# Performance work log

Hardware: AMD Instinct MI355X
Metric: run time of the kernel (lower is better)

Reference implementation:

```python
import jax, jax.numpy as jnp
import numpy as np

D = 256                      # covariance dim, hardcoded by bottleneck Conv2d(_, 256, 1)
ITER_N = 5                   # SqrtmLayer(output, 5)
_r, _c = np.triu_indices(D)
FLAT_IDX = jnp.asarray(_r * D + _c)   # upper-tri (incl. diag) indices into flattened d*d


def setup_inputs() -> dict:
    key = jax.random.key(0)
    ks = jax.random.split(key, 5)
    B, C, H, W = 64, 2048, 16, 16
    num_classes = 4
    feats = D * (D + 1) // 2  # 32896
    return {
        "features": jax.random.normal(ks[0], (B, C, H, W), jnp.float32),
        "w_bn": jax.random.normal(ks[1], (D, C), jnp.float32) * 0.02,
        "b_bn": jnp.zeros((D,), jnp.float32),
        "w_type": jax.random.normal(ks[2], (num_classes, feats), jnp.float32) * 0.01,
        "b_type": jnp.zeros((num_classes,), jnp.float32),
        "w_flag": jax.random.normal(ks[3], (1, feats), jnp.float32) * 0.01,
        "b_flag": jnp.zeros((1,), jnp.float32),
    }


def _covpool(x):
    # x: [B, d, h, w] -> second-order pooling: x_f @ I_hat @ x_f^T, equivalent
    # to (1/M) * centered @ centered^T  (I_hat = -1/M^2 * ones + 1/M * eye)
    B, d, h, w = x.shape
    M = h * w
    xf = x.reshape(B, d, M)
    centered = xf - xf.mean(axis=2, keepdims=True)
    return jnp.einsum('bim,bjm->bij', centered, centered) / M  # [B, d, d]


def _sqrtm_ns(A, iter_n=ITER_N):
    # Newton-Schulz iteration for matrix square root (iSQRT-COV style)
    B, d, _ = A.shape
    I3 = 3.0 * jnp.eye(d, dtype=A.dtype)
    normA = jnp.trace(A, axis1=1, axis2=2)          # [B], pre-normalization
    An = A / normA[:, None, None]
    ZY = 0.5 * (I3 - An)
    Y = jnp.matmul(An, ZY)
    Z = ZY
    for _ in range(iter_n - 2):
        ZY = 0.5 * (I3 - jnp.matmul(Z, Y))
        Y = jnp.matmul(Y, ZY)
        Z = jnp.matmul(ZY, Z)
    YZY = 0.5 * jnp.matmul(Y, I3 - jnp.matmul(Z, Y))
    return YZY * jnp.sqrt(normA)[:, None, None]     # post-compensation


def reference(features, w_bn, b_bn, w_type, b_type, w_flag, b_flag):
    # 1x1 bottleneck conv: [B, C, H, W] -> [B, 256, H, W]
    x = jnp.einsum('bchw,oc->bohw', features, w_bn) + b_bn[None, :, None, None]
    cov = _covpool(x)                # [B, 256, 256]
    s = _sqrtm_ns(cov)               # [B, 256, 256]
    B = s.shape[0]
    vec = s.reshape(B, D * D)[:, FLAT_IDX]   # triu-vec: [B, 32896]
    type_logits = vec @ w_type.T + b_type    # [B, num_classes]
    flag_logits = vec @ w_flag.T + b_flag    # [B, 1]
    return (type_logits, flag_logits)
```

## Files before the change

kernel.cpp:

```cpp
#include <hip/hip_runtime.h>
#include <math.h>


typedef __attribute__((ext_vector_type(8))) short bf16x8;
typedef __attribute__((ext_vector_type(4))) float f32x4;
typedef __attribute__((ext_vector_type(4))) unsigned u32x4;
typedef __attribute__((ext_vector_type(2))) unsigned u32x2;

enum { E_T = 0, E_TNS = 1, E_COV = 2, E_SF32 = 3 };

__device__ __forceinline__ unsigned fbits(float f) { union { float f; unsigned u; } x; x.f = f; return x.u; }
__device__ __forceinline__ float bitsf(unsigned u) { union { float f; unsigned u; } x; x.u = u; return x.f; }
__device__ __forceinline__ float bf16v(short h) { return bitsf(((unsigned)(unsigned short)h) << 16); }

__device__ __forceinline__ unsigned pack_h(float a, float b) {
  return (fbits(a) >> 16) | (fbits(b) & 0xFFFF0000u);
}
__device__ __forceinline__ unsigned pack_l(float a, float b) {
  float la = a - bitsf(fbits(a) & 0xFFFF0000u);
  float lb = b - bitsf(fbits(b) & 0xFFFF0000u);
  return (fbits(la) >> 16) | (fbits(lb) & 0xFFFF0000u);
}

__device__ __forceinline__ void gld16(const void* g, void* l) {
  __builtin_amdgcn_global_load_lds(
      (const __attribute__((address_space(1))) void*)(size_t)(g),
      (__attribute__((address_space(3))) void*)(unsigned)(size_t)(l), 16, 0, 0);
}

#define WAIT_VM(N) asm volatile("s_waitcnt vmcnt(" #N ")" ::: "memory")
#define BARRIER() do { __builtin_amdgcn_s_barrier(); asm volatile("" ::: "memory"); } while (0)

__global__ __launch_bounds__(256) void conv_k(
    const char* __restrict__ Wf, const float* __restrict__ F,
    char* __restrict__ X, const float* __restrict__ bias)
{
  __shared__ __align__(16) char lds[3 * 16384];
  const int tid = threadIdx.x, lane = tid & 63, w = tid >> 6;
  const int wr = w >> 1, wc = w & 1, fr = lane & 15, g = lane >> 4;
  const int bz = blockIdx.z, ib = blockIdx.y * 128, jb = blockIdx.x * 64;
  const float* Fb = F + (size_t)bz * 524288;

  f32x4 acc[4][2] = {};
  float xv[16];

  auto stageA = [&](int t) {
    const char* Ag = Wf + (size_t)t * 32768 + (size_t)ib * 128;
    char* lA = lds + (t % 3) * 16384;
#pragma unroll
    for (int i = 0; i < 4; ++i)
      gld16(Ag + (w + i * 4) * 1024 + lane * 16, lA + (w + i * 4) * 1024);
  };
  auto loadB = [&](int t) {
    const float* src = Fb + ((size_t)t * 32 + g * 8) * 256 + jb + wc * 32 + fr;
#pragma unroll
    for (int n = 0; n < 2; ++n)
#pragma unroll
      for (int e = 0; e < 8; ++e)
        xv[n * 8 + e] = src[e * 256 + n * 16];
  };

  stageA(0); stageA(1); loadB(0);

  for (int t = 0; t < 64; ++t) {
    if (t < 63) { WAIT_VM(20); } else { WAIT_VM(0); }
    BARRIER();
    if (t + 2 < 64) stageA(t + 2);
    bf16x8 bH[2], bL[2];
#pragma unroll
    for (int n = 0; n < 2; ++n) {
      short hh[8], ll[8];
#pragma unroll
      for (int e = 0; e < 8; ++e) {
        const float v = xv[n * 8 + e];
        const unsigned u = fbits(v);
        hh[e] = (short)(u >> 16);
        ll[e] = (short)(fbits(v - bitsf(u & 0xFFFF0000u)) >> 16);
      }
      bH[n] = *(bf16x8*)hh; bL[n] = *(bf16x8*)ll;
    }
    if (t + 1 < 64) loadB(t + 1);
    const char* lA = lds + (t % 3) * 16384;
    bf16x8 aH[4], aL[4];
#pragma unroll
    for (int m = 0; m < 4; ++m) {
      const int r = wr * 64 + m * 16 + fr;
      const char* p = lA + r * 128;
      aH[m] = *(const bf16x8*)(p + ((g ^ (r & 7)) << 4));
      aL[m] = *(const bf16x8*)(p + (((g + 4) ^ (r & 7)) << 4));
    }
#pragma unroll
    for (int m = 0; m < 4; ++m)
#pragma unroll
      for (int n = 0; n < 2; ++n) {
        f32x4 c = acc[m][n];
        c = __builtin_amdgcn_mfma_f32_16x16x32_bf16(aL[m], bH[n], c, 0, 0, 0);
        c = __builtin_amdgcn_mfma_f32_16x16x32_bf16(aH[m], bL[n], c, 0, 0, 0);
        c = __builtin_amdgcn_mfma_f32_16x16x32_bf16(aH[m], bH[n], c, 0, 0, 0);
        acc[m][n] = c;
      }
  }

  char* Xb = X + (size_t)bz * 262144;
#pragma unroll
  for (int m = 0; m < 4; ++m) {
    const int gi0 = ib + wr * 64 + m * 16 + g * 4;
#pragma unroll
    for (int n = 0; n < 2; ++n) {
      const int gj = jb + wc * 32 + n * 16 + fr;
      const int ktj = gj >> 5, sj = (gj & 31) >> 3, bo = (gj & 7) * 2;
#pragma unroll
      for (int j = 0; j < 4; ++j) {
        const int gi = gi0 + j;
        char* rp = Xb + (size_t)ktj * 32768 + (size_t)gi * 128;
        const float v = acc[m][n][j] + bias[gi];
        const unsigned u = fbits(v);
        *(short*)(rp + ((sj ^ (gi & 7)) << 4) + bo) = (short)(u >> 16);
        *(short*)(rp + (((sj + 4) ^ (gi & 7)) << 4) + bo) =
            (short)(fbits(v - bitsf(u & 0xFFFF0000u)) >> 16);
      }
    }
  }
}

template <int EPI, bool PAIR>
__global__ __launch_bounds__(128) void gemm_s(
    const char* __restrict__ A1, const char* __restrict__ B1, char* __restrict__ C1,
    const char* __restrict__ A2, const char* __restrict__ B2, char* __restrict__ C2,
    char* __restrict__ Cz, const float* __restrict__ mu,
    const float* __restrict__ nrm, float* __restrict__ Cf)
{
  static const int TIa[10] = {0, 0, 0, 0, 1, 1, 1, 2, 2, 3};
  static const int TJa[10] = {0, 1, 2, 3, 1, 2, 3, 2, 3, 3};
  __shared__ __align__(16) char lds[3 * 16384];
  const int tid = threadIdx.x, lane = tid & 63, w = tid >> 6;
  const int fr = lane & 15, g = lane >> 4;
  int bz = blockIdx.z;
  const char* Ab; const char* Bb; char* Cb;
  if (PAIR && bz >= 64) { bz -= 64; Ab = A2; Bb = B2; Cb = C2; }
  else { Ab = A1; Bb = B1; Cb = C1; }
  Ab += (size_t)bz * 262144; Bb += (size_t)bz * 262144; Cb += (size_t)bz * 262144;
  const int bi = TIa[blockIdx.x], bj = TJa[blockIdx.x];
  const int ib = bi * 64, jb = bj * 64;

  f32x4 acc[4][2] = {};

  auto stage = [&](int t) {
    char* lA = lds + (t % 3) * 16384;
    const char* Ag = Ab + (size_t)t * 32768 + (size_t)ib * 128;
    const char* Bg = Bb + (size_t)t * 32768 + (size_t)jb * 128;
#pragma unroll
    for (int i = 0; i < 8; ++i) {
      const int s = w + i * 2;
      if (s < 8) gld16(Ag + s * 1024 + lane * 16, lA + s * 1024);
      else       gld16(Bg + (s - 8) * 1024 + lane * 16, lA + 8192 + (s - 8) * 1024);
    }
  };

  stage(0); stage(1);
  for (int t = 0; t < 8; ++t) {
    if (t < 7) { WAIT_VM(8); } else { WAIT_VM(0); }
    BARRIER();
    if (t + 2 < 8) stage(t + 2);
    const char* lA = lds + (t % 3) * 16384;
    const char* lB = lA + 8192;
    bf16x8 aH[4], aL[4], bH[2], bL[2];
#pragma unroll
    for (int m = 0; m < 4; ++m) {
      const int r = m * 16 + fr;
      const char* p = lA + r * 128;
      aH[m] = *(const bf16x8*)(p + ((g ^ (r & 7)) << 4));
      aL[m] = *(const bf16x8*)(p + (((g + 4) ^ (r & 7)) << 4));
    }
#pragma unroll
    for (int n = 0; n < 2; ++n) {
      const int r = w * 32 + n * 16 + fr;
      const char* p = lB + r * 128;
      bH[n] = *(const bf16x8*)(p + ((g ^ (r & 7)) << 4));
      bL[n] = *(const bf16x8*)(p + (((g + 4) ^ (r & 7)) << 4));
    }
#pragma unroll
    for (int m = 0; m < 4; ++m)
#pragma unroll
      for (int n = 0; n < 2; ++n) {
        f32x4 c = acc[m][n];
        c = __builtin_amdgcn_mfma_f32_16x16x32_bf16(aL[m], bH[n], c, 0, 0, 0);
        c = __builtin_amdgcn_mfma_f32_16x16x32_bf16(aH[m], bL[n], c, 0, 0, 0);
        c = __builtin_amdgcn_mfma_f32_16x16x32_bf16(aH[m], bH[n], c, 0, 0, 0);
        acc[m][n] = c;
      }
  }

  const float sq = (EPI == E_SF32) ? sqrtf(nrm[bz]) : 0.f;
  const float rn = (EPI == E_COV) ? 1.0f / nrm[bz] : 0.f;

#pragma unroll
  for (int m = 0; m < 4; ++m) {
    const int gi0 = ib + m * 16 + g * 4;
#pragma unroll
    for (int n = 0; n < 2; ++n) {
      const int gj = jb + w * 32 + n * 16 + fr;
      float vv[4];
#pragma unroll
      for (int j = 0; j < 4; ++j) {
        float v = acc[m][n][j];
        if (EPI == E_COV)
          v = (v * (1.f / 256.f) - mu[bz * 256 + gi0 + j] * mu[bz * 256 + gj]) * rn;
        if (EPI == E_TNS) v = (gi0 + j == gj ? 1.5f : 0.f) - 0.5f * v;
        if (EPI == E_SF32) v = v * sq;
        vv[j] = v;
      }
      if (EPI == E_SF32) {
        *(f32x4*)(Cf + (size_t)bz * 65536 + (size_t)gj * 256 + gi0) =
            (f32x4){vv[0], vv[1], vv[2], vv[3]};
        if (bi != bj) {
#pragma unroll
          for (int j = 0; j < 4; ++j)
            Cf[(size_t)bz * 65536 + (size_t)(gi0 + j) * 256 + gj] = vv[j];
        }
      } else {
        const int kt = gi0 >> 5, s = (gi0 & 31) >> 3, bo = (gi0 & 7) * 2;
        char* rp = Cb + (size_t)kt * 32768 + (size_t)gj * 128;
        *(u32x2*)(rp + ((s ^ (gj & 7)) << 4) + bo) = (u32x2){pack_h(vv[0], vv[1]), pack_h(vv[2], vv[3])};
        *(u32x2*)(rp + (((s + 4) ^ (gj & 7)) << 4) + bo) = (u32x2){pack_l(vv[0], vv[1]), pack_l(vv[2], vv[3])};
        if (bi != bj) {
          const int kt2 = gj >> 5, s2 = (gj & 31) >> 3, bo2 = (gj & 7) * 2;
#pragma unroll
          for (int j = 0; j < 4; ++j) {
            const int gi = gi0 + j;
            char* rp2 = Cb + (size_t)kt2 * 32768 + (size_t)gi * 128;
            const unsigned u = fbits(vv[j]);
            *(short*)(rp2 + ((s2 ^ (gi & 7)) << 4) + bo2) = (short)(u >> 16);
            *(short*)(rp2 + (((s2 + 4) ^ (gi & 7)) << 4) + bo2) =
                (short)(fbits(vv[j] - bitsf(u & 0xFFFF0000u)) >> 16);
          }
        }
        if (EPI == E_COV) {
          float zz[4];
#pragma unroll
          for (int j = 0; j < 4; ++j) zz[j] = (gi0 + j == gj ? 1.5f : 0.f) - 0.5f * vv[j];
          char* zp = Cz + (size_t)bz * 262144 + (size_t)kt * 32768 + (size_t)gj * 128;
          *(u32x2*)(zp + ((s ^ (gj & 7)) << 4) + bo) = (u32x2){pack_h(zz[0], zz[1]), pack_h(zz[2], zz[3])};
          *(u32x2*)(zp + (((s + 4) ^ (gj & 7)) << 4) + bo) = (u32x2){pack_l(zz[0], zz[1]), pack_l(zz[2], zz[3])};
          if (bi != bj) {
            const int kt2 = gj >> 5, s2 = (gj & 31) >> 3, bo2 = (gj & 7) * 2;
#pragma unroll
            for (int j = 0; j < 4; ++j) {
              const int gi = gi0 + j;
              char* zp2 = Cz + (size_t)bz * 262144 + (size_t)kt2 * 32768 + (size_t)gi * 128;
              const unsigned u = fbits(zz[j]);
              *(short*)(zp2 + ((s2 ^ (gi & 7)) << 4) + bo2) = (short)(u >> 16);
              *(short*)(zp2 + (((s2 + 4) ^ (gi & 7)) << 4) + bo2) =
                  (short)(fbits(zz[j] - bitsf(u & 0xFFFF0000u)) >> 16);
            }
          }
        }
      }
    }
  }
}

__global__ __launch_bounds__(256) void cvt_w(const float* __restrict__ wsrc,
                                             char* __restrict__ Wf)
{
  const int kt = blockIdx.x, r = threadIdx.x;
  const float* src = wsrc + (size_t)r * 2048 + kt * 32;
  char* rp = Wf + (size_t)kt * 32768 + (size_t)r * 128;
#pragma unroll
  for (int s = 0; s < 4; ++s) {
    float x[8];
#pragma unroll
    for (int e = 0; e < 8; ++e) x[e] = src[s * 8 + e];
    *(u32x4*)(rp + ((s ^ (r & 7)) << 4)) =
        (u32x4){pack_h(x[0], x[1]), pack_h(x[2], x[3]), pack_h(x[4], x[5]), pack_h(x[6], x[7])};
    *(u32x4*)(rp + (((s + 4) ^ (r & 7)) << 4)) =
        (u32x4){pack_l(x[0], x[1]), pack_l(x[2], x[3]), pack_l(x[4], x[5]), pack_l(x[6], x[7])};
  }
}

__global__ __launch_bounds__(256) void build_w2(const float* __restrict__ w_type,
                                                const float* __restrict__ w_flag,
                                                float* __restrict__ W2)
{
  const int v = blockIdx.x >> 6, chunk = blockIdx.x & 63;
  const float* src = (v < 4) ? (w_type + (size_t)v * 32896) : w_flag;
  const int e0 = chunk * 1024 + threadIdx.x * 4;
#pragma unroll
  for (int q = 0; q < 4; ++q) {
    const int e = e0 + q;
    const int i = e >> 8, j = e & 255;
    const int r = i < j ? i : j, c = i < j ? j : i;
    const int t = r * 256 - (r * (r - 1)) / 2 + (c - r);
    W2[(size_t)v * 65536 + e] = src[t] * (i == j ? 1.0f : 0.5f);
  }
}

__global__ __launch_bounds__(256) void meanvar(const char* __restrict__ X,
                                               float* __restrict__ mu,
                                               float* __restrict__ nrm)
{
  const int b = blockIdx.x, i = threadIdx.x;
  const char* rp0 = X + (size_t)b * 262144 + (size_t)i * 128;
  float s = 0.f, ss = 0.f;
  for (int kt = 0; kt < 8; ++kt) {
    const char* rp = rp0 + kt * 32768;
#pragma unroll
    for (int sl = 0; sl < 4; ++sl) {
      bf16x8 h8 = *(const bf16x8*)(rp + ((sl ^ (i & 7)) << 4));
      bf16x8 l8 = *(const bf16x8*)(rp + (((sl + 4) ^ (i & 7)) << 4));
#pragma unroll
      for (int e = 0; e < 8; ++e) {
        const float v = bf16v(h8[e]) + bf16v(l8[e]);
        s += v; ss += v * v;
      }
    }
  }
  const float m = s * (1.f / 256.f);
  mu[b * 256 + i] = m;
  __shared__ float red[256];
  red[i] = ss * (1.f / 256.f) - m * m;
  __syncthreads();
  for (int o = 128; o > 0; o >>= 1) {
    if (i < o) red[i] += red[i + o];
    __syncthreads();
  }
  if (i == 0) nrm[b] = red[0];
}

__global__ __launch_bounds__(256) void head2(
    const float* __restrict__ Sf, const float* __restrict__ W2,
    const float* __restrict__ b_type, const float* __restrict__ b_flag,
    float* __restrict__ out)
{
  const int b = blockIdx.x, v = blockIdx.y, tid = threadIdx.x;
  const float4* s4 = (const float4*)(Sf + (size_t)b * 65536);
  const float4* w4 = (const float4*)(W2 + (size_t)v * 65536);
  float acc = 0.f;
  for (int i = tid; i < 16384; i += 256) {
    const float4 a = s4[i], c = w4[i];
    acc += a.x * c.x + a.y * c.y + a.z * c.z + a.w * c.w;
  }
  __shared__ float red[256];
  red[tid] = acc;
  __syncthreads();
  for (int o = 128; o > 0; o >>= 1) {
    if (tid < o) red[tid] += red[tid + o];
    __syncthreads();
  }
  if (tid == 0) {
    if (v < 4) out[b * 4 + v] = red[0] + b_type[v];
    else       out[256 + b] = red[0] + b_flag[0];
  }
}

extern "C" void kernel_launch(void* const* d_in, const int* in_sizes, int n_in,
                              void* d_out, int out_size, void* d_ws, size_t ws_size,
                              hipStream_t stream)
{
  const float* features = (const float*)d_in[0];
  const float* w_bn     = (const float*)d_in[1];
  const float* b_bn     = (const float*)d_in[2];
  const float* w_type   = (const float*)d_in[3];
  const float* b_type   = (const float*)d_in[4];
  const float* w_flag   = (const float*)d_in[5];
  const float* b_flag   = (const float*)d_in[6];
  float* out = (float*)d_out;

  char* W = (char*)d_ws;
  const size_t PB = 16777216;
  char* P0 = W;           char* P1 = W + PB;     char* P2 = W + 2 * PB;
  char* P3 = W + 3 * PB;  char* P4 = W + 4 * PB;
  char* Wf = W + 5 * PB;
  float* W2 = (float*)Wf;
  float* mu = (float*)(W + 5 * PB + 2097152);
  float* nrm = mu + 64 * 256;
  float* Sf = (float*)P4;

  const dim3 tgrid(10, 1, 64), tgrid2(10, 1, 128), tb(128);

  cvt_w<<<dim3(64), dim3(256), 0, stream>>>(w_bn, Wf);
  conv_k<<<dim3(4, 2, 64), dim3(256), 0, stream>>>(Wf, features, P0, b_bn);
  build_w2<<<dim3(320), dim3(256), 0, stream>>>(w_type, w_flag, W2);
  meanvar<<<dim3(64), dim3(256), 0, stream>>>(P0, mu, nrm);

  gemm_s<E_COV, false><<<tgrid, tb, 0, stream>>>(
      P0, P0, P1, nullptr, nullptr, nullptr, P2, mu, nrm, nullptr);
  gemm_s<E_T, false><<<tgrid, tb, 0, stream>>>(
      P1, P2, P3, nullptr, nullptr, nullptr, nullptr, nullptr, nullptr, nullptr);
  gemm_s<E_TNS, false><<<tgrid, tb, 0, stream>>>(
      P2, P3, P4, nullptr, nullptr, nullptr, nullptr, nullptr, nullptr, nullptr);
  gemm_s<E_T, true><<<tgrid2, tb, 0, stream>>>(
      P3, P4, P0, P4, P2, P1, nullptr, nullptr, nullptr, nullptr);
  gemm_s<E_TNS, false><<<tgrid, tb, 0, stream>>>(
      P1, P0, P2, nullptr, nullptr, nullptr, nullptr, nullptr, nullptr, nullptr);
  gemm_s<E_T, true><<<tgrid2, tb, 0, stream>>>(
      P0, P2, P3, P2, P1, P4, nullptr, nullptr, nullptr, nullptr);
  gemm_s<E_TNS, false><<<tgrid, tb, 0, stream>>>(
      P4, P3, P0, nullptr, nullptr, nullptr, nullptr, nullptr, nullptr, nullptr);
  gemm_s<E_T, true><<<tgrid2, tb, 0, stream>>>(
      P3, P0, P1, P0, P4, P2, nullptr, nullptr, nullptr, nullptr);
  gemm_s<E_TNS, false><<<tgrid, tb, 0, stream>>>(
      P2, P1, P3, nullptr, nullptr, nullptr, nullptr, nullptr, nullptr, nullptr);
  gemm_s<E_SF32, false><<<tgrid, tb, 0, stream>>>(
      P1, P3, nullptr, nullptr, nullptr, nullptr, nullptr, nullptr, nrm, Sf);

  head2<<<dim3(64, 5), dim3(256), 0, stream>>>(Sf, W2, b_type, b_flag, out);
  (void)in_sizes; (void)n_in; (void)out_size; (void)ws_size;
}
```

Before: 335.6 us.

## Fuse Newton-Schulz steps into column-block kernels with direct register fragment loads

```diff
diff --git a/kernel.cpp b/kernel.cpp
--- a/kernel.cpp
+++ b/kernel.cpp
@@ -7,8 +7,6 @@
 typedef __attribute__((ext_vector_type(4))) unsigned u32x4;
 typedef __attribute__((ext_vector_type(2))) unsigned u32x2;
 
-enum { E_T = 0, E_TNS = 1, E_COV = 2, E_SF32 = 3 };
-
 __device__ __forceinline__ unsigned fbits(float f) { union { float f; unsigned u; } x; x.f = f; return x.u; }
 __device__ __forceinline__ float bitsf(unsigned u) { union { float f; unsigned u; } x; x.u = u; return x.f; }
 __device__ __forceinline__ float bf16v(short h) { return bitsf(((unsigned)(unsigned short)h) << 16); }
@@ -22,83 +20,125 @@
   return (fbits(la) >> 16) | (fbits(lb) & 0xFFFF0000u);
 }
 
-__device__ __forceinline__ void gld16(const void* g, void* l) {
-  __builtin_amdgcn_global_load_lds(
-      (const __attribute__((address_space(1))) void*)(size_t)(g),
-      (__attribute__((address_space(3))) void*)(unsigned)(size_t)(l), 16, 0, 0);
-}
-
-#define WAIT_VM(N) asm volatile("s_waitcnt vmcnt(" #N ")" ::: "memory")
-#define BARRIER() do { __builtin_amdgcn_s_barrier(); asm volatile("" ::: "memory"); } while (0)
+__device__ __forceinline__ const bf16x8* fragp(const char* M, int kt, int row,
+                                               int g, int pl) {
+  return (const bf16x8*)(M + (size_t)kt * 32768 + (size_t)row * 128 +
+                         ((((pl << 2) + g) ^ (row & 7)) << 4));
+}
+__device__ __forceinline__ const bf16x8* fragl(const char* L, int kt, int row,
+                                               int g, int pl) {
+  return (const bf16x8*)(L + kt * 8192 + row * 128 +
+                         ((((pl << 2) + g) ^ (row & 7)) << 4));
+}
+
+__device__ __forceinline__ void write_quad_g(char* M, int row, int k0,
+                                             const float* v) {
+  char* rp = M + (size_t)(k0 >> 5) * 32768 + (size_t)row * 128;
+  const int s = (k0 & 31) >> 3, bo = (k0 & 7) * 2;
+  *(u32x2*)(rp + (((s) ^ (row & 7)) << 4) + bo) =
+      (u32x2){pack_h(v[0], v[1]), pack_h(v[2], v[3])};
+  *(u32x2*)(rp + (((s + 4) ^ (row & 7)) << 4) + bo) =
+      (u32x2){pack_l(v[0], v[1]), pack_l(v[2], v[3])};
+}
+__device__ __forceinline__ void write_quad_l(char* L, int row, int k0,
+                                             const float* v) {
+  char* rp = L + (k0 >> 5) * 8192 + row * 128;
+  const int s = (k0 & 31) >> 3, bo = (k0 & 7) * 2;
+  *(u32x2*)(rp + (((s) ^ (row & 7)) << 4) + bo) =
+      (u32x2){pack_h(v[0], v[1]), pack_h(v[2], v[3])};
+  *(u32x2*)(rp + (((s + 4) ^ (row & 7)) << 4) + bo) =
+      (u32x2){pack_l(v[0], v[1]), pack_l(v[2], v[3])};
+}
+__device__ __forceinline__ void read_quad_g(const char* M, int row, int k0,
+                                            float* v) {
+  const char* rp = M + (size_t)(k0 >> 5) * 32768 + (size_t)row * 128;
+  const int s = (k0 & 31) >> 3, bo = (k0 & 7) * 2;
+  const u32x2 hq = *(const u32x2*)(rp + (((s) ^ (row & 7)) << 4) + bo);
+  const u32x2 lq = *(const u32x2*)(rp + (((s + 4) ^ (row & 7)) << 4) + bo);
+  v[0] = bitsf(hq[0] << 16) + bitsf(lq[0] << 16);
+  v[1] = bitsf(hq[0] & 0xFFFF0000u) + bitsf(lq[0] & 0xFFFF0000u);
+  v[2] = bitsf(hq[1] << 16) + bitsf(lq[1] << 16);
+  v[3] = bitsf(hq[1] & 0xFFFF0000u) + bitsf(lq[1] & 0xFFFF0000u);
+}
+
+#define MFMA3(c, aH, aL, bH, bL)                                            \
+  c = __builtin_amdgcn_mfma_f32_16x16x32_bf16(aL, bH, c, 0, 0, 0);          \
+  c = __builtin_amdgcn_mfma_f32_16x16x32_bf16(aH, bL, c, 0, 0, 0);          \
+  c = __builtin_amdgcn_mfma_f32_16x16x32_bf16(aH, bH, c, 0, 0, 0);
 
 __global__ __launch_bounds__(256) void conv_k(
     const char* __restrict__ Wf, const float* __restrict__ F,
     char* __restrict__ X, const float* __restrict__ bias)
 {
-  __shared__ __align__(16) char lds[3 * 16384];
   const int tid = threadIdx.x, lane = tid & 63, w = tid >> 6;
   const int wr = w >> 1, wc = w & 1, fr = lane & 15, g = lane >> 4;
   const int bz = blockIdx.z, ib = blockIdx.y * 128, jb = blockIdx.x * 64;
   const float* Fb = F + (size_t)bz * 524288;
 
   f32x4 acc[4][2] = {};
-  float xv[16];
-
-  auto stageA = [&](int t) {
-    const char* Ag = Wf + (size_t)t * 32768 + (size_t)ib * 128;
-    char* lA = lds + (t % 3) * 16384;
-#pragma unroll
-    for (int i = 0; i < 4; ++i)
-      gld16(Ag + (w + i * 4) * 1024 + lane * 16, lA + (w + i * 4) * 1024);
-  };
-  auto loadB = [&](int t) {
-    const float* src = Fb + ((size_t)t * 32 + g * 8) * 256 + jb + wc * 32 + fr;
+  bf16x8 pa[2][4][2];
+  float xv[2][16];
+
+#pragma unroll
+  for (int par = 0; par < 2; ++par) {
+#pragma unroll
+    for (int m = 0; m < 4; ++m) {
+      const int r = ib + wr * 64 + m * 16 + fr;
+#pragma unroll
+      for (int pl = 0; pl < 2; ++pl) pa[par][m][pl] = *fragp(Wf, par, r, g, pl);
+    }
+    const float* src = Fb + ((size_t)par * 32 + g * 8) * 256 + jb + wc * 32 + fr;
 #pragma unroll
     for (int n = 0; n < 2; ++n)
 #pragma unroll
-      for (int e = 0; e < 8; ++e)
-        xv[n * 8 + e] = src[e * 256 + n * 16];
-  };
-
-  stageA(0); stageA(1); loadB(0);
-
-  for (int t = 0; t < 64; ++t) {
-    if (t < 63) { WAIT_VM(20); } else { WAIT_VM(0); }
-    BARRIER();
-    if (t + 2 < 64) stageA(t + 2);
-    bf16x8 bH[2], bL[2];
-#pragma unroll
-    for (int n = 0; n < 2; ++n) {
-      short hh[8], ll[8];
-#pragma unroll
-      for (int e = 0; e < 8; ++e) {
-        const float v = xv[n * 8 + e];
-        const unsigned u = fbits(v);
-        hh[e] = (short)(u >> 16);
-        ll[e] = (short)(fbits(v - bitsf(u & 0xFFFF0000u)) >> 16);
-      }
-      bH[n] = *(bf16x8*)hh; bL[n] = *(bf16x8*)ll;
-    }
-    if (t + 1 < 64) loadB(t + 1);
-    const char* lA = lds + (t % 3) * 16384;
-    bf16x8 aH[4], aL[4];
-#pragma unroll
-    for (int m = 0; m < 4; ++m) {
-      const int r = wr * 64 + m * 16 + fr;
-      const char* p = lA + r * 128;
-      aH[m] = *(const bf16x8*)(p + ((g ^ (r & 7)) << 4));
-      aL[m] = *(const bf16x8*)(p + (((g + 4) ^ (r & 7)) << 4));
-    }
-#pragma unroll
-    for (int m = 0; m < 4; ++m)
+      for (int e = 0; e < 8; ++e) xv[par][n * 8 + e] = src[e * 256 + n * 16];
+  }
+
+  for (int t2 = 0; t2 < 64; t2 += 2) {
+#pragma unroll
+    for (int par = 0; par < 2; ++par) {
+      const int t = t2 + par;
+      bf16x8 aH[4], aL[4];
+#pragma unroll
+      for (int m = 0; m < 4; ++m) { aH[m] = pa[par][m][0]; aL[m] = pa[par][m][1]; }
+      bf16x8 bH[2], bL[2];
 #pragma unroll
       for (int n = 0; n < 2; ++n) {
-        f32x4 c = acc[m][n];
-        c = __builtin_amdgcn_mfma_f32_16x16x32_bf16(aL[m], bH[n], c, 0, 0, 0);
-        c = __builtin_amdgcn_mfma_f32_16x16x32_bf16(aH[m], bL[n], c, 0, 0, 0);
-        c = __builtin_amdgcn_mfma_f32_16x16x32_bf16(aH[m], bH[n], c, 0, 0, 0);
-        acc[m][n] = c;
-      }
+        short hh[8], ll[8];
+#pragma unroll
+        for (int e = 0; e < 8; ++e) {
+          const float v = xv[par][n * 8 + e];
+          const unsigned u = fbits(v);
+          hh[e] = (short)(u >> 16);
+          ll[e] = (short)(fbits(v - bitsf(u & 0xFFFF0000u)) >> 16);
+        }
+        bH[n] = *(bf16x8*)hh; bL[n] = *(bf16x8*)ll;
+      }
+      if (t + 2 < 64) {
+#pragma unroll
+        for (int m = 0; m < 4; ++m) {
+          const int r = ib + wr * 64 + m * 16 + fr;
+#pragma unroll
+          for (int pl = 0; pl < 2; ++pl)
+            pa[par][m][pl] = *fragp(Wf, t + 2, r, g, pl);
+        }
+        const float* src =
+            Fb + ((size_t)(t + 2) * 32 + g * 8) * 256 + jb + wc * 32 + fr;
+#pragma unroll
+        for (int n = 0; n < 2; ++n)
+#pragma unroll
+          for (int e = 0; e < 8; ++e)
+            xv[par][n * 8 + e] = src[e * 256 + n * 16];
+      }
+#pragma unroll
+      for (int m = 0; m < 4; ++m)
+#pragma unroll
+        for (int n = 0; n < 2; ++n) {
+          f32x4 c = acc[m][n];
+          MFMA3(c, aH[m], aL[m], bH[n], bL[n]);
+          acc[m][n] = c;
+        }
+    }
   }
 
   char* Xb = X + (size_t)bz * 262144;
@@ -123,137 +163,225 @@
   }
 }
 
-template <int EPI, bool PAIR>
-__global__ __launch_bounds__(128) void gemm_s(
-    const char* __restrict__ A1, const char* __restrict__ B1, char* __restrict__ C1,
-    const char* __restrict__ A2, const char* __restrict__ B2, char* __restrict__ C2,
-    char* __restrict__ Cz, const float* __restrict__ mu,
-    const float* __restrict__ nrm, float* __restrict__ Cf)
-{
-  static const int TIa[10] = {0, 0, 0, 0, 1, 1, 1, 2, 2, 3};
-  static const int TJa[10] = {0, 1, 2, 3, 1, 2, 3, 2, 3, 3};
-  __shared__ __align__(16) char lds[3 * 16384];
+template <int MODE>
+__global__ __launch_bounds__(512) void col_k(
+    const char* __restrict__ A1, const char* __restrict__ Bsrc,
+    const char* __restrict__ Ys, const char* __restrict__ Zs,
+    char* __restrict__ outA, char* __restrict__ outB,
+    const float* __restrict__ mu, const float* __restrict__ nrm,
+    float* __restrict__ Sf)
+{
+  __shared__ __align__(16) char Plds[65536];
   const int tid = threadIdx.x, lane = tid & 63, w = tid >> 6;
   const int fr = lane & 15, g = lane >> 4;
-  int bz = blockIdx.z;
-  const char* Ab; const char* Bb; char* Cb;
-  if (PAIR && bz >= 64) { bz -= 64; Ab = A2; Bb = B2; Cb = C2; }
-  else { Ab = A1; Bb = B1; Cb = C1; }
-  Ab += (size_t)bz * 262144; Bb += (size_t)bz * 262144; Cb += (size_t)bz * 262144;
-  const int bi = TIa[blockIdx.x], bj = TJa[blockIdx.x];
-  const int ib = bi * 64, jb = bj * 64;
-
-  f32x4 acc[4][2] = {};
-
-  auto stage = [&](int t) {
-    char* lA = lds + (t % 3) * 16384;
-    const char* Ag = Ab + (size_t)t * 32768 + (size_t)ib * 128;
-    const char* Bg = Bb + (size_t)t * 32768 + (size_t)jb * 128;
-#pragma unroll
-    for (int i = 0; i < 8; ++i) {
-      const int s = w + i * 2;
-      if (s < 8) gld16(Ag + s * 1024 + lane * 16, lA + s * 1024);
-      else       gld16(Bg + (s - 8) * 1024 + lane * 16, lA + 8192 + (s - 8) * 1024);
-    }
-  };
-
-  stage(0); stage(1);
-  for (int t = 0; t < 8; ++t) {
-    if (t < 7) { WAIT_VM(8); } else { WAIT_VM(0); }
-    BARRIER();
-    if (t + 2 < 8) stage(t + 2);
-    const char* lA = lds + (t % 3) * 16384;
-    const char* lB = lA + 8192;
-    bf16x8 aH[4], aL[4], bH[2], bL[2];
-#pragma unroll
-    for (int m = 0; m < 4; ++m) {
-      const int r = m * 16 + fr;
-      const char* p = lA + r * 128;
-      aH[m] = *(const bf16x8*)(p + ((g ^ (r & 7)) << 4));
-      aL[m] = *(const bf16x8*)(p + (((g + 4) ^ (r & 7)) << 4));
-    }
-#pragma unroll
-    for (int n = 0; n < 2; ++n) {
-      const int r = w * 32 + n * 16 + fr;
-      const char* p = lB + r * 128;
-      bH[n] = *(const bf16x8*)(p + ((g ^ (r & 7)) << 4));
-      bL[n] = *(const bf16x8*)(p + (((g + 4) ^ (r & 7)) << 4));
-    }
-#pragma unroll
-    for (int m = 0; m < 4; ++m)
-#pragma unroll
-      for (int n = 0; n < 2; ++n) {
-        f32x4 c = acc[m][n];
-        c = __builtin_amdgcn_mfma_f32_16x16x32_bf16(aL[m], bH[n], c, 0, 0, 0);
-        c = __builtin_amdgcn_mfma_f32_16x16x32_bf16(aH[m], bL[n], c, 0, 0, 0);
-        c = __builtin_amdgcn_mfma_f32_16x16x32_bf16(aH[m], bH[n], c, 0, 0, 0);
-        acc[m][n] = c;
-      }
-  }
-
-  const float sq = (EPI == E_SF32) ? sqrtf(nrm[bz]) : 0.f;
-  const float rn = (EPI == E_COV) ? 1.0f / nrm[bz] : 0.f;
-
-#pragma unroll
-  for (int m = 0; m < 4; ++m) {
-    const int gi0 = ib + m * 16 + g * 4;
-#pragma unroll
-    for (int n = 0; n < 2; ++n) {
-      const int gj = jb + w * 32 + n * 16 + fr;
-      float vv[4];
-#pragma unroll
-      for (int j = 0; j < 4; ++j) {
-        float v = acc[m][n][j];
-        if (EPI == E_COV)
-          v = (v * (1.f / 256.f) - mu[bz * 256 + gi0 + j] * mu[bz * 256 + gj]) * rn;
-        if (EPI == E_TNS) v = (gi0 + j == gj ? 1.5f : 0.f) - 0.5f * v;
-        if (EPI == E_SF32) v = v * sq;
-        vv[j] = v;
-      }
-      if (EPI == E_SF32) {
-        *(f32x4*)(Cf + (size_t)bz * 65536 + (size_t)gj * 256 + gi0) =
-            (f32x4){vv[0], vv[1], vv[2], vv[3]};
-        if (bi != bj) {
-#pragma unroll
-          for (int j = 0; j < 4; ++j)
-            Cf[(size_t)bz * 65536 + (size_t)(gi0 + j) * 256 + gj] = vv[j];
-        }
-      } else {
-        const int kt = gi0 >> 5, s = (gi0 & 31) >> 3, bo = (gi0 & 7) * 2;
-        char* rp = Cb + (size_t)kt * 32768 + (size_t)gj * 128;
-        *(u32x2*)(rp + ((s ^ (gj & 7)) << 4) + bo) = (u32x2){pack_h(vv[0], vv[1]), pack_h(vv[2], vv[3])};
-        *(u32x2*)(rp + (((s + 4) ^ (gj & 7)) << 4) + bo) = (u32x2){pack_l(vv[0], vv[1]), pack_l(vv[2], vv[3])};
-        if (bi != bj) {
-          const int kt2 = gj >> 5, s2 = (gj & 31) >> 3, bo2 = (gj & 7) * 2;
-#pragma unroll
-          for (int j = 0; j < 4; ++j) {
-            const int gi = gi0 + j;
-            char* rp2 = Cb + (size_t)kt2 * 32768 + (size_t)gi * 128;
-            const unsigned u = fbits(vv[j]);
-            *(short*)(rp2 + ((s2 ^ (gi & 7)) << 4) + bo2) = (short)(u >> 16);
-            *(short*)(rp2 + (((s2 + 4) ^ (gi & 7)) << 4) + bo2) =
-                (short)(fbits(vv[j] - bitsf(u & 0xFFFF0000u)) >> 16);
+  const int blk = blockIdx.x;
+  const int bz = (blk & 7) * 8 + ((blk >> 3) & 7);
+  const int jb = (blk >> 6) * 64;
+  const size_t MB = 262144;
+  const char* Ab = A1 + (size_t)bz * MB;
+  const char* Bb = Bsrc + (size_t)bz * MB;
+  const int r0 = g * 4;
+
+  f32x4 acc[2][4] = {};
+  {
+    bf16x8 pa[2][2][2], pb[2][4][2];
+#pragma unroll
+    for (int par = 0; par < 2; ++par) {
+#pragma unroll
+      for (int m = 0; m < 2; ++m) {
+        const int r = w * 32 + m * 16 + fr;
+#pragma unroll
+        for (int pl = 0; pl < 2; ++pl) pa[par][m][pl] = *fragp(Ab, par, r, g, pl);
+      }
+#pragma unroll
+      for (int n = 0; n < 4; ++n) {
+        const int r = jb + n * 16 + fr;
+#pragma unroll
+        for (int pl = 0; pl < 2; ++pl) pb[par][n][pl] = *fragp(Bb, par, r, g, pl);
+      }
+    }
+    for (int t2 = 0; t2 < 8; t2 += 2) {
+#pragma unroll
+      for (int par = 0; par < 2; ++par) {
+        const int t = t2 + par;
+        bf16x8 aH[2], aL[2], bH[4], bL[4];
+#pragma unroll
+        for (int m = 0; m < 2; ++m) { aH[m] = pa[par][m][0]; aL[m] = pa[par][m][1]; }
+#pragma unroll
+        for (int n = 0; n < 4; ++n) { bH[n] = pb[par][n][0]; bL[n] = pb[par][n][1]; }
+        if (t + 2 < 8) {
+#pragma unroll
+          for (int m = 0; m < 2; ++m) {
+            const int r = w * 32 + m * 16 + fr;
+#pragma unroll
+            for (int pl = 0; pl < 2; ++pl)
+              pa[par][m][pl] = *fragp(Ab, t + 2, r, g, pl);
           }
-        }
-        if (EPI == E_COV) {
-          float zz[4];
-#pragma unroll
-          for (int j = 0; j < 4; ++j) zz[j] = (gi0 + j == gj ? 1.5f : 0.f) - 0.5f * vv[j];
-          char* zp = Cz + (size_t)bz * 262144 + (size_t)kt * 32768 + (size_t)gj * 128;
-          *(u32x2*)(zp + ((s ^ (gj & 7)) << 4) + bo) = (u32x2){pack_h(zz[0], zz[1]), pack_h(zz[2], zz[3])};
-          *(u32x2*)(zp + (((s + 4) ^ (gj & 7)) << 4) + bo) = (u32x2){pack_l(zz[0], zz[1]), pack_l(zz[2], zz[3])};
-          if (bi != bj) {
-            const int kt2 = gj >> 5, s2 = (gj & 31) >> 3, bo2 = (gj & 7) * 2;
-#pragma unroll
-            for (int j = 0; j < 4; ++j) {
-              const int gi = gi0 + j;
-              char* zp2 = Cz + (size_t)bz * 262144 + (size_t)kt2 * 32768 + (size_t)gi * 128;
-              const unsigned u = fbits(zz[j]);
-              *(short*)(zp2 + ((s2 ^ (gi & 7)) << 4) + bo2) = (short)(u >> 16);
-              *(short*)(zp2 + (((s2 + 4) ^ (gi & 7)) << 4) + bo2) =
-                  (short)(fbits(zz[j] - bitsf(u & 0xFFFF0000u)) >> 16);
+#pragma unroll
+          for (int n = 0; n < 4; ++n) {
+            const int r = jb + n * 16 + fr;
+#pragma unroll
+            for (int pl = 0; pl < 2; ++pl)
+              pb[par][n][pl] = *fragp(Bb, t + 2, r, g, pl);
+          }
+        }
+#pragma unroll
+        for (int m = 0; m < 2; ++m)
+#pragma unroll
+          for (int n = 0; n < 4; ++n) {
+            f32x4 c = acc[m][n];
+            MFMA3(c, aH[m], aL[m], bH[n], bL[n]);
+            acc[m][n] = c;
+          }
+      }
+    }
+  }
+
+  if constexpr (MODE == 0) {
+    const float rn = 1.0f / nrm[bz];
+    const float* mub = mu + bz * 256;
+    char* oA = outA + (size_t)bz * MB;
+    char* oB = outB + (size_t)bz * MB;
+#pragma unroll
+    for (int m = 0; m < 2; ++m) {
+      const int gi0 = w * 32 + m * 16 + r0;
+#pragma unroll
+      for (int n = 0; n < 4; ++n) {
+        const int gj = jb + n * 16 + fr;
+        float vv[4], zz[4];
+#pragma unroll
+        for (int j = 0; j < 4; ++j) {
+          const float v =
+              (acc[m][n][j] * (1.f / 256.f) - mub[gi0 + j] * mub[gj]) * rn;
+          vv[j] = v;
+          zz[j] = (gi0 + j == gj ? 1.5f : 0.f) - 0.5f * v;
+        }
+        write_quad_g(oA, gj, gi0, vv);
+        write_quad_g(oB, gj, gi0, zz);
+      }
+    }
+  } else if constexpr (MODE == 1) {
+    char* oA = outA + (size_t)bz * MB;
+#pragma unroll
+    for (int m = 0; m < 2; ++m) {
+      const int gi0 = w * 32 + m * 16 + r0;
+#pragma unroll
+      for (int n = 0; n < 4; ++n) {
+        const int gj = jb + n * 16 + fr;
+        float av[4], vv[4];
+        read_quad_g(Bb, gj, gi0, av);
+#pragma unroll
+        for (int j = 0; j < 4; ++j) vv[j] = 1.5f * av[j] - 0.5f * acc[m][n][j];
+        write_quad_g(oA, gj, gi0, vv);
+      }
+    }
+  } else {
+#pragma unroll
+    for (int m = 0; m < 2; ++m) {
+      const int gi0 = w * 32 + m * 16 + r0;
+#pragma unroll
+      for (int n = 0; n < 4; ++n) {
+        const int jl = n * 16 + fr;
+        float vv[4] = {acc[m][n][0], acc[m][n][1], acc[m][n][2], acc[m][n][3]};
+        write_quad_l(Plds, jl, gi0, vv);
+      }
+    }
+    __syncthreads();
+
+    const char* Yb = Ys + (size_t)bz * MB;
+    const char* Zb = (MODE == 2) ? (Zs + (size_t)bz * MB) : nullptr;
+    f32x4 aY[2][4] = {}, aZ[2][4] = {};
+    bf16x8 py[2][2][2], pz[2][2][2];
+#pragma unroll
+    for (int par = 0; par < 2; ++par)
+#pragma unroll
+      for (int m = 0; m < 2; ++m) {
+        const int r = w * 32 + m * 16 + fr;
+#pragma unroll
+        for (int pl = 0; pl < 2; ++pl) {
+          py[par][m][pl] = *fragp(Yb, par, r, g, pl);
+          if constexpr (MODE == 2) pz[par][m][pl] = *fragp(Zb, par, r, g, pl);
+        }
+      }
+    for (int t2 = 0; t2 < 8; t2 += 2) {
+#pragma unroll
+      for (int par = 0; par < 2; ++par) {
+        const int t = t2 + par;
+        bf16x8 yH[2], yL[2], zH[2], zL[2];
+#pragma unroll
+        for (int m = 0; m < 2; ++m) {
+          yH[m] = py[par][m][0]; yL[m] = py[par][m][1];
+          if constexpr (MODE == 2) { zH[m] = pz[par][m][0]; zL[m] = pz[par][m][1]; }
+        }
+        if (t + 2 < 8) {
+#pragma unroll
+          for (int m = 0; m < 2; ++m) {
+            const int r = w * 32 + m * 16 + fr;
+#pragma unroll
+            for (int pl = 0; pl < 2; ++pl) {
+              py[par][m][pl] = *fragp(Yb, t + 2, r, g, pl);
+              if constexpr (MODE == 2) pz[par][m][pl] = *fragp(Zb, t + 2, r, g, pl);
             }
           }
+        }
+        bf16x8 bH[4], bL[4];
+#pragma unroll
+        for (int n = 0; n < 4; ++n) {
+          const int jl = n * 16 + fr;
+          bH[n] = *fragl(Plds, t, jl, g, 0);
+          bL[n] = *fragl(Plds, t, jl, g, 1);
+        }
+#pragma unroll
+        for (int m = 0; m < 2; ++m)
+#pragma unroll
+          for (int n = 0; n < 4; ++n) {
+            f32x4 cy = aY[m][n];
+            MFMA3(cy, yH[m], yL[m], bH[n], bL[n]);
+            aY[m][n] = cy;
+            if constexpr (MODE == 2) {
+              f32x4 cz = aZ[m][n];
+              MFMA3(cz, zH[m], zL[m], bH[n], bL[n]);
+              aZ[m][n] = cz;
+            }
+          }
+      }
+    }
+    if constexpr (MODE == 2) {
+      char* oA = outA + (size_t)bz * MB;
+      char* oB = outB + (size_t)bz * MB;
+#pragma unroll
+      for (int m = 0; m < 2; ++m) {
+        const int gi0 = w * 32 + m * 16 + r0;
+#pragma unroll
+        for (int n = 0; n < 4; ++n) {
+          const int gj = jb + n * 16 + fr;
+          float base[4], vv[4];
+          read_quad_g(Yb, gj, gi0, base);
+#pragma unroll
+          for (int j = 0; j < 4; ++j) vv[j] = 1.5f * base[j] - 0.5f * aY[m][n][j];
+          write_quad_g(oA, gj, gi0, vv);
+          read_quad_g(Zb, gj, gi0, base);
+#pragma unroll
+          for (int j = 0; j < 4; ++j) vv[j] = 1.5f * base[j] - 0.5f * aZ[m][n][j];
+          write_quad_g(oB, gj, gi0, vv);
+        }
+      }
+    } else {
+      const float sq = sqrtf(nrm[bz]);
+      float* Sb = Sf + (size_t)bz * 65536;
+#pragma unroll
+      for (int m = 0; m < 2; ++m) {
+        const int gi0 = w * 32 + m * 16 + r0;
+#pragma unroll
+        for (int n = 0; n < 4; ++n) {
+          const int gj = jb + n * 16 + fr;
+          float base[4];
+          read_quad_g(Yb, gj, gi0, base);
+          f32x4 vv;
+#pragma unroll
+          for (int j = 0; j < 4; ++j)
+            vv[j] = (1.5f * base[j] - 0.5f * aY[m][n][j]) * sq;
+          *(f32x4*)(Sb + (size_t)gj * 256 + gi0) = vv;
         }
       }
     }
@@ -376,33 +504,18 @@
   float* nrm = mu + 64 * 256;
   float* Sf = (float*)P4;
 
-  const dim3 tgrid(10, 1, 64), tgrid2(10, 1, 128), tb(128);
-
   cvt_w<<<dim3(64), dim3(256), 0, stream>>>(w_bn, Wf);
   conv_k<<<dim3(4, 2, 64), dim3(256), 0, stream>>>(Wf, features, P0, b_bn);
   build_w2<<<dim3(320), dim3(256), 0, stream>>>(w_type, w_flag, W2);
   meanvar<<<dim3(64), dim3(256), 0, stream>>>(P0, mu, nrm);
 
-  gemm_s<E_COV, false><<<tgrid, tb, 0, stream>>>(
-      P0, P0, P1, nullptr, nullptr, nullptr, P2, mu, nrm, nullptr);
-  gemm_s<E_T, false><<<tgrid, tb, 0, stream>>>(
-      P1, P2, P3, nullptr, nullptr, nullptr, nullptr, nullptr, nullptr, nullptr);
-  gemm_s<E_TNS, false><<<tgrid, tb, 0, stream>>>(
-      P2, P3, P4, nullptr, nullptr, nullptr, nullptr, nullptr, nullptr, nullptr);
-  gemm_s<E_T, true><<<tgrid2, tb, 0, stream>>>(
-      P3, P4, P0, P4, P2, P1, nullptr, nullptr, nullptr, nullptr);
-  gemm_s<E_TNS, false><<<tgrid, tb, 0, stream>>>(
-      P1, P0, P2, nullptr, nullptr, nullptr, nullptr, nullptr, nullptr, nullptr);
-  gemm_s<E_T, true><<<tgrid2, tb, 0, stream>>>(
-      P0, P2, P3, P2, P1, P4, nullptr, nullptr, nullptr, nullptr);
-  gemm_s<E_TNS, false><<<tgrid, tb, 0, stream>>>(
-      P4, P3, P0, nullptr, nullptr, nullptr, nullptr, nullptr, nullptr, nullptr);
-  gemm_s<E_T, true><<<tgrid2, tb, 0, stream>>>(
-      P3, P0, P1, P0, P4, P2, nullptr, nullptr, nullptr, nullptr);
-  gemm_s<E_TNS, false><<<tgrid, tb, 0, stream>>>(
-      P2, P1, P3, nullptr, nullptr, nullptr, nullptr, nullptr, nullptr, nullptr);
-  gemm_s<E_SF32, false><<<tgrid, tb, 0, stream>>>(
-      P1, P3, nullptr, nullptr, nullptr, nullptr, nullptr, nullptr, nrm, Sf);
+  const dim3 cg(256), cb(512);
+  col_k<0><<<cg, cb, 0, stream>>>(P0, P0, nullptr, nullptr, P1, P2, mu, nrm, nullptr);
+  col_k<1><<<cg, cb, 0, stream>>>(P1, P1, nullptr, nullptr, P3, nullptr, nullptr, nullptr, nullptr);
+  col_k<2><<<cg, cb, 0, stream>>>(P2, P3, P3, P2, P0, P4, nullptr, nullptr, nullptr);
+  col_k<2><<<cg, cb, 0, stream>>>(P4, P0, P0, P4, P1, P2, nullptr, nullptr, nullptr);
+  col_k<2><<<cg, cb, 0, stream>>>(P2, P1, P1, P2, P3, P0, nullptr, nullptr, nullptr);
+  col_k<3><<<cg, cb, 0, stream>>>(P0, P3, P3, nullptr, nullptr, nullptr, nullptr, nrm, Sf);
 
   head2<<<dim3(64, 5), dim3(256), 0, stream>>>(Sf, W2, b_type, b_flag, out);
   (void)in_sizes; (void)n_in; (void)out_size; (void)ws_size;
```

Result: faster. 280.2 us (-16.5%).
